# Kernel tuning notes

Hardware: AMD Instinct MI355X
Metric: run time of the kernel (lower is better)

Reference implementation:

```python
import jax, jax.numpy as jnp
import numpy as np

B, W, H, C = 8, 32, 32, 64   # batch, width, height, hidden_size
NH = 8                        # num_attention_heads
M = 32                        # max_position_embeddings
P = C // 2                    # position_embedding_size (query_positional_score=True)


def setup_inputs() -> dict:
    key = jax.random.key(0)
    ks = jax.random.split(key, 7)
    s = 0.02
    return {
        "hidden_states": jax.random.normal(ks[0], (B, W, H, C), dtype=jnp.float32),
        "row_emb": jax.random.normal(ks[1], (2 * M - 1, P), dtype=jnp.float32) * s,
        "col_emb": jax.random.normal(ks[2], (2 * M - 1, P), dtype=jnp.float32) * s,
        "Wq": jax.random.normal(ks[3], (NH * C, C), dtype=jnp.float32) * s,
        "bq": jnp.zeros((NH * C,), dtype=jnp.float32),
        "Wk": jax.random.normal(ks[4], (NH * C, C), dtype=jnp.float32) * s,
        "bk": jnp.zeros((NH * C,), dtype=jnp.float32),
        "Wv": jax.random.normal(ks[5], (C, NH * C), dtype=jnp.float32) * s,
        "bv": jnp.zeros((C,), dtype=jnp.float32),
    }


def reference(hidden_states, row_emb, col_emb, Wq, bq, Wk, bk, Wv, bv):
    b, w, h, c = hidden_states.shape
    nh = Wq.shape[0] // c
    half = c // 2
    center = row_emb.shape[0] // 2  # = max_position_embeddings - 1

    # projections: all_head_size = nh * c (per source: hidden_size * num_heads)
    q = (hidden_states @ Wq.T + bq).reshape(b, w, h, nh, c)
    k = (hidden_states @ Wk.T + bk).reshape(b, w, h, nh, c)

    # relative index tables: rel[i, j] = (j - i) + (M - 1)
    iw = jnp.arange(w)
    ih = jnp.arange(h)
    rel_w = iw[None, :] - iw[:, None] + center   # (w, w)
    rel_h = ih[None, :] - ih[:, None] + center   # (h, h)
    r_emb = row_emb[rel_w]  # (w, w, P)
    c_emb = col_emb[rel_h]  # (h, h, P)

    # positional scores: q split into row/col halves
    q_row = q[..., :half]
    q_col = q[..., half:]
    row_scores = jnp.einsum('bijhd,ikd->bijhk', q_row, r_emb)  # (b,w,h,nh,w)
    col_scores = jnp.einsum('bijhd,jld->bijhl', q_col, c_emb)  # (b,w,h,nh,h)
    scale = jnp.sqrt(jnp.asarray(c, dtype=hidden_states.dtype))
    scores = (row_scores[..., :, None] + col_scores[..., None, :]) / scale  # (b,w,h,nh,w,h)

    # content scores q^T k
    scores = scores + jnp.einsum('bijhd,bklhd->bijhkl', q, k) / scale

    # softmax over merged spatial key dims (k,l)
    probs = jax.nn.softmax(scores.reshape(b, w, h, nh, w * h), axis=-1).reshape(scores.shape)

    # value mixing directly with hidden_states, then output projection
    mixed = jnp.einsum('bijhkl,bkld->bijhd', probs, hidden_states).reshape(b, w, h, nh * c)
    return mixed @ Wv.T + bv
```

## Files before the change

kernel.cpp:

```cpp
#include <hip/hip_runtime.h>
#include <math.h>

typedef __bf16 bf16;
typedef bf16 bf16x2 __attribute__((ext_vector_type(2)));
typedef bf16 bf16x4 __attribute__((ext_vector_type(4)));
typedef bf16 bf16x8 __attribute__((ext_vector_type(8)));
typedef float f32x4 __attribute__((ext_vector_type(4)));

constexpr int CENTER = 31;
constexpr float QSCALE = 0.125f * 1.4426950408889634f;

static __device__ __forceinline__ unsigned short f2bf_bits(float f) {
    bf16 b = (bf16)f;
    return __builtin_bit_cast(unsigned short, b);
}

static __device__ __forceinline__ float fast_exp2(float x) {
#if __has_builtin(__builtin_amdgcn_exp2f)
    return __builtin_amdgcn_exp2f(x);
#else
    return exp2f(x);
#endif
}

__global__ __launch_bounds__(256)
void prep_kernel(const float* __restrict__ hid,
                 const float* __restrict__ Wq, const float* __restrict__ Wk,
                 const float* __restrict__ Wv,
                 bf16* __restrict__ hb, bf16* __restrict__ htb,
                 bf16* __restrict__ Wqb, bf16* __restrict__ Wkb,
                 bf16* __restrict__ Wvp)
{
    __shared__ __attribute__((aligned(16))) bf16 hs[64][72];

    const int t   = threadIdx.x;
    const int blk = blockIdx.x;
    const int b   = blk >> 4, kc = blk & 15;

    {
        int row = t >> 2, c4 = (t & 3) * 16;
        const float4* src = (const float4*)(hid + ((size_t)b * 1024 + kc * 64 + row) * 64 + c4);
        bf16 tmp[16];
        #pragma unroll
        for (int u = 0; u < 4; ++u) {
            float4 v = src[u];
            tmp[4*u+0] = (bf16)v.x; tmp[4*u+1] = (bf16)v.y;
            tmp[4*u+2] = (bf16)v.z; tmp[4*u+3] = (bf16)v.w;
        }
        *(int4*)&hs[row][c4]     = ((int4*)tmp)[0];
        *(int4*)&hs[row][c4 + 8] = ((int4*)tmp)[1];
        bf16* hdst = hb + ((size_t)b * 1024 + kc * 64 + row) * 64 + c4;
        *(int4*)hdst       = ((int4*)tmp)[0];
        *(int4*)(hdst + 8) = ((int4*)tmp)[1];
    }

    {
        int idx = blk * 256 + t;
        if (idx < 8192) {
            float4 vq = ((const float4*)Wq)[idx];
            float4 vk = ((const float4*)Wk)[idx];
            float4 vv = ((const float4*)Wv)[idx];
            ushort4 pq, pk2, pv;
            pq.x = f2bf_bits(vq.x); pq.y = f2bf_bits(vq.y); pq.z = f2bf_bits(vq.z); pq.w = f2bf_bits(vq.w);
            pk2.x = f2bf_bits(vk.x); pk2.y = f2bf_bits(vk.y); pk2.z = f2bf_bits(vk.z); pk2.w = f2bf_bits(vk.w);
            pv.x = f2bf_bits(vv.x); pv.y = f2bf_bits(vv.y); pv.z = f2bf_bits(vv.z); pv.w = f2bf_bits(vv.w);
            ((ushort4*)Wqb)[idx] = pq;
            ((ushort4*)Wkb)[idx] = pk2;
            int c = idx >> 7, o4 = (idx & 127) * 4;
            size_t dst = (size_t)((c >> 4) * 16 + (o4 >> 5)) * 512 + (c & 15) * 32 + (o4 & 31);
            *(ushort4*)(Wvp + dst) = pv;
        }
    }
    __syncthreads();

    {
        int d = t >> 2, p0 = (t & 3) * 16;
        ushort tmp[16];
        #pragma unroll
        for (int i = 0; i < 16; ++i)
            tmp[i] = __builtin_bit_cast(unsigned short, hs[p0 + i][d]);
        bf16* dst = htb + ((size_t)b * 64 + d) * 1024 + kc * 64 + p0;
        *(int4*)dst       = ((int4*)tmp)[0];
        *(int4*)(dst + 8) = ((int4*)tmp)[1];
    }
}

__global__ __launch_bounds__(256)
void qkproj_kernel(const bf16* __restrict__ hb,
                   const bf16* __restrict__ Wqb, const float* __restrict__ bq,
                   const bf16* __restrict__ Wkb, const float* __restrict__ bk,
                   bf16* __restrict__ qb, bf16* __restrict__ kb)
{
    __shared__ __attribute__((aligned(16))) bf16 As[128][72];
    __shared__ __attribute__((aligned(16))) bf16 Bs[128][72];

    const int t  = threadIdx.x;
    const int pt = blockIdx.x;
    const int ot = blockIdx.y;
    const int z  = blockIdx.z;
    const int p0 = pt * 128;
    const int b  = p0 >> 10;

    const bf16* Wb        = z ? Wkb : Wqb;
    const float* bias     = z ? bk : bq;
    bf16* outp            = z ? kb : qb;
    const float scale     = z ? 1.0f : QSCALE;

    {
        int row = t >> 1, ch = (t & 1) * 32;
        const int4* asrc = (const int4*)(hb + (size_t)(p0 + row) * 64 + ch);
        const int4* bsrc = (const int4*)(Wb + (size_t)(ot * 128 + row) * 64 + ch);
        #pragma unroll
        for (int u = 0; u < 4; ++u) {
            *(int4*)&As[row][ch + u * 8] = asrc[u];
            *(int4*)&Bs[row][ch + u * 8] = bsrc[u];
        }
    }
    __syncthreads();

    const int w = t >> 6, ln = t & 63, l15 = ln & 15, quad = ln >> 4;

    bf16x8 a[2][2];
    #pragma unroll
    for (int mt = 0; mt < 2; ++mt) {
        a[mt][0] = *(const bf16x8*)&As[w * 32 + mt * 16 + l15][quad * 8];
        a[mt][1] = *(const bf16x8*)&As[w * 32 + mt * 16 + l15][32 + quad * 8];
    }

    const f32x4 z4 = {0.f, 0.f, 0.f, 0.f};
    f32x4 acc[2][8];
    #pragma unroll
    for (int mt = 0; mt < 2; ++mt)
        #pragma unroll
        for (int nt = 0; nt < 8; ++nt) acc[mt][nt] = z4;

    #pragma unroll
    for (int nt = 0; nt < 8; ++nt) {
        bf16x8 b0 = *(const bf16x8*)&Bs[nt * 16 + l15][quad * 8];
        bf16x8 b1 = *(const bf16x8*)&Bs[nt * 16 + l15][32 + quad * 8];
        #pragma unroll
        for (int mt = 0; mt < 2; ++mt) {
            acc[mt][nt] = __builtin_amdgcn_mfma_f32_16x16x32_bf16(a[mt][0], b0, acc[mt][nt], 0, 0, 0);
            acc[mt][nt] = __builtin_amdgcn_mfma_f32_16x16x32_bf16(a[mt][1], b1, acc[mt][nt], 0, 0, 0);
        }
    }

    #pragma unroll
    for (int nt = 0; nt < 8; ++nt) {
        int o = ot * 128 + nt * 16 + l15;
        float bv = bias[o];
        int hh = o >> 6, d = o & 63;
        #pragma unroll
        for (int mt = 0; mt < 2; ++mt)
            #pragma unroll
            for (int r = 0; r < 4; ++r) {
                int pos = (p0 & 1023) + w * 32 + mt * 16 + quad * 4 + r;
                float val = (acc[mt][nt][r] + bv) * scale;
                outp[(((size_t)b * 8 + hh) * 1024 + pos) * 64 + d] = (bf16)val;
            }
    }
}

__global__ __launch_bounds__(256)
void bias_kernel(const bf16* __restrict__ qb,
                 const float* __restrict__ row_emb, const float* __restrict__ col_emb,
                 bf16* __restrict__ rowbias, bf16* __restrict__ colbias)
{
    __shared__ __attribute__((aligned(16))) bf16 embRs[63][40];
    __shared__ __attribute__((aligned(16))) bf16 embCs[63][40];

    const int t  = threadIdx.x;
    const int bh = blockIdx.x;
    const int sg = blockIdx.y;

    for (int i = t; i < 2016; i += 256) embRs[i >> 5][i & 31] = (bf16)row_emb[i];
    for (int i = t; i < 2016; i += 256) embCs[i >> 5][i & 31] = (bf16)col_emb[i];
    __syncthreads();

    const int w = t >> 6, ln = t & 63, l15 = ln & 15, quad = ln >> 4;

    #pragma unroll
    for (int u = 0; u < 2; ++u) {
        int s = sg * 8 + u * 4 + w;
        bool cm = s >= 32;
        int ij = cm ? s - 32 : s;

        bf16x8 a[2];
        #pragma unroll
        for (int mt = 0; mt < 2; ++mt) {
            const bf16* ap = cm
                ? qb + ((size_t)bh * 1024 + (mt * 16 + l15) * 32 + ij) * 64 + 32 + quad * 8
                : qb + ((size_t)bh * 1024 + ij * 32 + mt * 16 + l15) * 64 + quad * 8;
            a[mt] = *(const bf16x8*)ap;
        }
        bf16* ob = cm ? colbias : rowbias;

        #pragma unroll
        for (int nt = 0; nt < 2; ++nt) {
            int erow = nt * 16 + l15 + CENTER - ij;
            bf16x8 bfrag = cm ? *(const bf16x8*)&embCs[erow][quad * 8]
                              : *(const bf16x8*)&embRs[erow][quad * 8];
            #pragma unroll
            for (int mt = 0; mt < 2; ++mt) {
                f32x4 c = {0.f, 0.f, 0.f, 0.f};
                c = __builtin_amdgcn_mfma_f32_16x16x32_bf16(a[mt], bfrag, c, 0, 0, 0);
                #pragma unroll
                for (int r = 0; r < 4; ++r) {
                    int ql = mt * 16 + quad * 4 + r;
                    int qrow = cm ? ql * 32 + ij : ij * 32 + ql;
                    ob[((size_t)bh * 1024 + qrow) * 32 + nt * 16 + l15] = (bf16)c[r];
                }
            }
        }
    }
}

__global__ __launch_bounds__(256, 2)
void attn_kernel(const bf16* __restrict__ qb, const bf16* __restrict__ kb,
                 const bf16* __restrict__ htb,
                 const bf16* __restrict__ rowbias, const bf16* __restrict__ colbias,
                 bf16* __restrict__ mixedb)
{
    __shared__ __attribute__((aligned(16))) bf16 Ks[2][64][72];
    __shared__ __attribute__((aligned(16))) bf16 Hts[2][64][72];
    __shared__ __attribute__((aligned(16))) bf16 Pp[4][32][72];

    const int t  = threadIdx.x;
    const int id = blockIdx.x;
    const int r8 = id & 7;
    const int g  = id >> 3;
    const int qt = g & 7;
    const int bh = r8 * 8 + (g >> 3);
    const int b  = bh >> 3, h = bh & 7;
    const int q0 = qt * 128;
    const int w = t >> 6, ln = t & 63, l15 = ln & 15, quad = ln >> 4;

    bf16x8 bq_[2][2];
    float  cbv[2][2][4];
    const bf16* rbp[2];
    #pragma unroll
    for (int mt = 0; mt < 2; ++mt) {
        int qrow = q0 + w * 32 + mt * 16 + l15;
        const bf16* qp = qb + ((size_t)bh * 1024 + qrow) * 64;
        bq_[mt][0] = *(const bf16x8*)(qp + quad * 8);
        bq_[mt][1] = *(const bf16x8*)(qp + 32 + quad * 8);
        #pragma unroll
        for (int par = 0; par < 2; ++par) {
            bf16x4 cv = *(const bf16x4*)(colbias + ((size_t)bh * 1024 + qrow) * 32 + par * 16 + quad * 4);
            #pragma unroll
            for (int r = 0; r < 4; ++r) cbv[mt][par][r] = (float)cv[r];
        }
        rbp[mt] = rowbias + ((size_t)bh * 1024 + qrow) * 32;
    }

    const f32x4 z4 = {0.f, 0.f, 0.f, 0.f};
    f32x4 oacc[2][4];
    float lsum[2] = {0.f, 0.f};
    #pragma unroll
    for (int mt = 0; mt < 2; ++mt)
        #pragma unroll
        for (int dt = 0; dt < 4; ++dt) oacc[mt][dt] = z4;

    bf16* Pw = &Pp[w][0][0];
    const bf16* kcbase = kb + (size_t)bh * 1024 * 64;
    const bf16* hcbase = htb + (size_t)b * 64 * 1024;

    const int srow = t >> 2, sc = (t & 3) << 4;
    const bf16* kptr = kcbase + (size_t)srow * 64 + sc;
    const bf16* hptr = hcbase + (size_t)srow * 1024 + sc;

    int4 kr0 = *(const int4*)(kptr);
    int4 kr1 = *(const int4*)(kptr + 8);
    int4 hr0 = *(const int4*)(hptr);
    int4 hr1 = *(const int4*)(hptr + 8);
    *(int4*)&Ks[0][srow][sc]       = kr0;
    *(int4*)&Ks[0][srow][sc + 8]   = kr1;
    *(int4*)&Hts[0][srow][sc]      = hr0;
    *(int4*)&Hts[0][srow][sc + 8]  = hr1;
    kr0 = *(const int4*)(kptr + 4096);
    kr1 = *(const int4*)(kptr + 4096 + 8);
    hr0 = *(const int4*)(hptr + 64);
    hr1 = *(const int4*)(hptr + 64 + 8);
    bf16x2 rnext[2];
    #pragma unroll
    for (int mt = 0; mt < 2; ++mt) rnext[mt] = *(const bf16x2*)(rbp[mt]);
    __syncthreads();

    int cur = 0;
    for (int kc = 0; kc < 16; ++kc) {
        if (kc < 15) {
            *(int4*)&Ks[cur ^ 1][srow][sc]      = kr0;
            *(int4*)&Ks[cur ^ 1][srow][sc + 8]  = kr1;
            *(int4*)&Hts[cur ^ 1][srow][sc]     = hr0;
            *(int4*)&Hts[cur ^ 1][srow][sc + 8] = hr1;
        }
        float rb[2][2];
        #pragma unroll
        for (int mt = 0; mt < 2; ++mt) {
            rb[mt][0] = (float)rnext[mt][0];
            rb[mt][1] = (float)rnext[mt][1];
        }
        if (kc < 14) {
            const bf16* kn = kptr + (size_t)(kc + 2) * 4096;
            const bf16* hn = hptr + (size_t)(kc + 2) * 64;
            kr0 = *(const int4*)(kn);
            kr1 = *(const int4*)(kn + 8);
            hr0 = *(const int4*)(hn);
            hr1 = *(const int4*)(hn + 8);
        }
        if (kc < 15) {
            #pragma unroll
            for (int mt = 0; mt < 2; ++mt)
                rnext[mt] = *(const bf16x2*)(rbp[mt] + (kc + 1) * 2);
        }

        const bf16 (* __restrict__ Kc)[72]  = Ks[cur];
        const bf16 (* __restrict__ Hc)[72]  = Hts[cur];
        f32x4 sf[2][4];
        #pragma unroll
        for (int mt = 0; mt < 2; ++mt)
            #pragma unroll
            for (int kt = 0; kt < 4; ++kt) sf[mt][kt] = z4;
        __builtin_amdgcn_s_setprio(1);
        #pragma unroll
        for (int kt = 0; kt < 4; ++kt) {
            bf16x8 aK0 = *(const bf16x8*)&Kc[kt * 16 + l15][quad * 8];
            bf16x8 aK1 = *(const bf16x8*)&Kc[kt * 16 + l15][32 + quad * 8];
            #pragma unroll
            for (int mt = 0; mt < 2; ++mt) {
                sf[mt][kt] = __builtin_amdgcn_mfma_f32_16x16x32_bf16(aK0, bq_[mt][0], sf[mt][kt], 0, 0, 0);
                sf[mt][kt] = __builtin_amdgcn_mfma_f32_16x16x32_bf16(aK1, bq_[mt][1], sf[mt][kt], 0, 0, 0);
            }
        }
        __builtin_amdgcn_s_setprio(0);

        #pragma unroll
        for (int mt = 0; mt < 2; ++mt)
            #pragma unroll
            for (int kt = 0; kt < 4; ++kt) {
                float rbv = rb[mt][kt >> 1];
                ushort4 pk;
                float p0 = fast_exp2(sf[mt][kt][0] + rbv + cbv[mt][kt & 1][0]);
                float p1 = fast_exp2(sf[mt][kt][1] + rbv + cbv[mt][kt & 1][1]);
                float p2 = fast_exp2(sf[mt][kt][2] + rbv + cbv[mt][kt & 1][2]);
                float p3 = fast_exp2(sf[mt][kt][3] + rbv + cbv[mt][kt & 1][3]);
                lsum[mt] += (p0 + p1) + (p2 + p3);
                pk.x = f2bf_bits(p0); pk.y = f2bf_bits(p1);
                pk.z = f2bf_bits(p2); pk.w = f2bf_bits(p3);
                *(ushort4*)&Pw[(mt * 16 + l15) * 72 + kt * 16 + quad * 4] = pk;
            }

        bf16x8 bp[2][2];
        #pragma unroll
        for (int mt = 0; mt < 2; ++mt) {
            bp[mt][0] = *(const bf16x8*)&Pw[(mt * 16 + l15) * 72 + quad * 8];
            bp[mt][1] = *(const bf16x8*)&Pw[(mt * 16 + l15) * 72 + 32 + quad * 8];
        }
        __builtin_amdgcn_s_setprio(1);
        #pragma unroll
        for (int dt = 0; dt < 4; ++dt) {
            bf16x8 aH0 = *(const bf16x8*)&Hc[dt * 16 + l15][quad * 8];
            bf16x8 aH1 = *(const bf16x8*)&Hc[dt * 16 + l15][32 + quad * 8];
            #pragma unroll
            for (int mt = 0; mt < 2; ++mt) {
                oacc[mt][dt] = __builtin_amdgcn_mfma_f32_16x16x32_bf16(aH0, bp[mt][0], oacc[mt][dt], 0, 0, 0);
                oacc[mt][dt] = __builtin_amdgcn_mfma_f32_16x16x32_bf16(aH1, bp[mt][1], oacc[mt][dt], 0, 0, 0);
            }
        }
        __builtin_amdgcn_s_setprio(0);

        __syncthreads();
        cur ^= 1;
    }

    float inv[2];
    #pragma unroll
    for (int mt = 0; mt < 2; ++mt) {
        float v = lsum[mt];
        v += __shfl_xor(v, 16);
        v += __shfl_xor(v, 32);
        inv[mt] = 1.0f / v;
    }
    #pragma unroll
    for (int mt = 0; mt < 2; ++mt) {
        int pos = q0 + w * 32 + mt * 16 + l15;
        bf16* mb = mixedb + ((size_t)b * 1024 + pos) * 512 + h * 64;
        #pragma unroll
        for (int dt = 0; dt < 4; ++dt) {
            ushort4 pk;
            pk.x = f2bf_bits(oacc[mt][dt][0] * inv[mt]);
            pk.y = f2bf_bits(oacc[mt][dt][1] * inv[mt]);
            pk.z = f2bf_bits(oacc[mt][dt][2] * inv[mt]);
            pk.w = f2bf_bits(oacc[mt][dt][3] * inv[mt]);
            *(ushort4*)(mb + dt * 16 + quad * 4) = pk;
        }
    }
}

__global__ __launch_bounds__(256)
void out_proj_kernel(const bf16* __restrict__ mixedb,
                     const bf16* __restrict__ Wvp, const float* __restrict__ bv,
                     float* __restrict__ out)
{
    const int t  = threadIdx.x;
    const int p0 = blockIdx.x * 32;
    const int w = t >> 6, ln = t & 63, l15 = ln & 15, quad = ln >> 4;

    float bvv = bv[w * 16 + l15];
    f32x4 acc[2] = {(f32x4){bvv, bvv, bvv, bvv}, (f32x4){bvv, bvv, bvv, bvv}};

    const bf16* arow0 = mixedb + (size_t)(p0 + l15) * 512 + quad * 8;
    const bf16* arow1 = mixedb + (size_t)(p0 + 16 + l15) * 512 + quad * 8;
    const bf16* bbase = Wvp + (size_t)w * 16 * 512 + l15 * 32 + quad * 8;

    #pragma unroll
    for (int kc = 0; kc < 16; ++kc) {
        bf16x8 a0 = *(const bf16x8*)(arow0 + kc * 32);
        bf16x8 a1 = *(const bf16x8*)(arow1 + kc * 32);
        bf16x8 bfrag = *(const bf16x8*)(bbase + kc * 512);
        acc[0] = __builtin_amdgcn_mfma_f32_16x16x32_bf16(a0, bfrag, acc[0], 0, 0, 0);
        acc[1] = __builtin_amdgcn_mfma_f32_16x16x32_bf16(a1, bfrag, acc[1], 0, 0, 0);
    }

    #pragma unroll
    for (int mt = 0; mt < 2; ++mt)
        #pragma unroll
        for (int r = 0; r < 4; ++r)
            out[(size_t)(p0 + mt * 16 + quad * 4 + r) * 64 + w * 16 + l15] = acc[mt][r];
}

extern "C" void kernel_launch(void* const* d_in, const int* in_sizes, int n_in,
                              void* d_out, int out_size, void* d_ws, size_t ws_size,
                              hipStream_t stream)
{
    const float* hid     = (const float*)d_in[0];
    const float* row_emb = (const float*)d_in[1];
    const float* col_emb = (const float*)d_in[2];
    const float* Wq      = (const float*)d_in[3];
    const float* bq      = (const float*)d_in[4];
    const float* Wk      = (const float*)d_in[5];
    const float* bk      = (const float*)d_in[6];
    const float* Wv      = (const float*)d_in[7];
    const float* bv      = (const float*)d_in[8];
    float* out = (float*)d_out;

    bf16* qb      = (bf16*)d_ws;
    bf16* kb      = qb + (size_t)64 * 1024 * 64;
    bf16* htb     = kb + (size_t)64 * 1024 * 64;
    bf16* rowbias = htb + (size_t)8 * 64 * 1024;
    bf16* colbias = rowbias + (size_t)64 * 1024 * 32;
    bf16* mixedb  = colbias + (size_t)64 * 1024 * 32;
    bf16* hb      = mixedb + (size_t)8 * 1024 * 512;
    bf16* Wqb     = hb + (size_t)8 * 1024 * 64;
    bf16* Wkb     = Wqb + (size_t)512 * 64;
    bf16* Wvp     = Wkb + (size_t)512 * 64;

    prep_kernel<<<128, 256, 0, stream>>>(hid, Wq, Wk, Wv, hb, htb, Wqb, Wkb, Wvp);
    qkproj_kernel<<<dim3(64, 4, 2), 256, 0, stream>>>(hb, Wqb, bq, Wkb, bk, qb, kb);
    bias_kernel<<<dim3(64, 8), 256, 0, stream>>>(qb, row_emb, col_emb, rowbias, colbias);
    attn_kernel<<<512, 256, 0, stream>>>(qb, kb, htb, rowbias, colbias, mixedb);
    out_proj_kernel<<<256, 256, 0, stream>>>(mixedb, Wvp, bv, out);
}
```

Measured before the change: 131.3 us.

## Fuse prep and QK projection kernels, seed MFMA accumulators with bias

Merges the fp32-to-bf16 prep kernel into the QK projection kernel. Projection blocks now read fp32 hidden states and weights directly and convert them while staging into shared memory. Extra blocks in the same grid build the transposed hidden tensor and the packed Wv. This removes one launch and the intermediate bf16 hb/Wqb/Wkb buffers, but projection blocks now read twice as many input bytes. Separately, the attention kernel starts its score accumulators at the row and column bias, which removes the adds before exp2.

```diff
diff --git a/kernel.cpp b/kernel.cpp
--- a/kernel.cpp
+++ b/kernel.cpp
@@ -24,96 +24,91 @@
 }
 
 __global__ __launch_bounds__(256)
-void prep_kernel(const float* __restrict__ hid,
-                 const float* __restrict__ Wq, const float* __restrict__ Wk,
-                 const float* __restrict__ Wv,
-                 bf16* __restrict__ hb, bf16* __restrict__ htb,
-                 bf16* __restrict__ Wqb, bf16* __restrict__ Wkb,
-                 bf16* __restrict__ Wvp)
+void prep_qkproj_kernel(const float* __restrict__ hid,
+                        const float* __restrict__ Wq, const float* __restrict__ bq,
+                        const float* __restrict__ Wk, const float* __restrict__ bk,
+                        const float* __restrict__ Wv,
+                        bf16* __restrict__ qb, bf16* __restrict__ kb,
+                        bf16* __restrict__ htb, bf16* __restrict__ Wvp)
 {
-    __shared__ __attribute__((aligned(16))) bf16 hs[64][72];
-
-    const int t   = threadIdx.x;
-    const int blk = blockIdx.x;
-    const int b   = blk >> 4, kc = blk & 15;
-
-    {
-        int row = t >> 2, c4 = (t & 3) * 16;
-        const float4* src = (const float4*)(hid + ((size_t)b * 1024 + kc * 64 + row) * 64 + c4);
-        bf16 tmp[16];
-        #pragma unroll
-        for (int u = 0; u < 4; ++u) {
-            float4 v = src[u];
-            tmp[4*u+0] = (bf16)v.x; tmp[4*u+1] = (bf16)v.y;
-            tmp[4*u+2] = (bf16)v.z; tmp[4*u+3] = (bf16)v.w;
-        }
-        *(int4*)&hs[row][c4]     = ((int4*)tmp)[0];
-        *(int4*)&hs[row][c4 + 8] = ((int4*)tmp)[1];
-        bf16* hdst = hb + ((size_t)b * 1024 + kc * 64 + row) * 64 + c4;
-        *(int4*)hdst       = ((int4*)tmp)[0];
-        *(int4*)(hdst + 8) = ((int4*)tmp)[1];
-    }
-
-    {
-        int idx = blk * 256 + t;
-        if (idx < 8192) {
-            float4 vq = ((const float4*)Wq)[idx];
-            float4 vk = ((const float4*)Wk)[idx];
-            float4 vv = ((const float4*)Wv)[idx];
-            ushort4 pq, pk2, pv;
-            pq.x = f2bf_bits(vq.x); pq.y = f2bf_bits(vq.y); pq.z = f2bf_bits(vq.z); pq.w = f2bf_bits(vq.w);
-            pk2.x = f2bf_bits(vk.x); pk2.y = f2bf_bits(vk.y); pk2.z = f2bf_bits(vk.z); pk2.w = f2bf_bits(vk.w);
-            pv.x = f2bf_bits(vv.x); pv.y = f2bf_bits(vv.y); pv.z = f2bf_bits(vv.z); pv.w = f2bf_bits(vv.w);
-            ((ushort4*)Wqb)[idx] = pq;
-            ((ushort4*)Wkb)[idx] = pk2;
-            int c = idx >> 7, o4 = (idx & 127) * 4;
-            size_t dst = (size_t)((c >> 4) * 16 + (o4 >> 5)) * 512 + (c & 15) * 32 + (o4 & 31);
-            *(ushort4*)(Wvp + dst) = pv;
-        }
-    }
-    __syncthreads();
-
-    {
-        int d = t >> 2, p0 = (t & 3) * 16;
-        ushort tmp[16];
-        #pragma unroll
-        for (int i = 0; i < 16; ++i)
-            tmp[i] = __builtin_bit_cast(unsigned short, hs[p0 + i][d]);
-        bf16* dst = htb + ((size_t)b * 64 + d) * 1024 + kc * 64 + p0;
-        *(int4*)dst       = ((int4*)tmp)[0];
-        *(int4*)(dst + 8) = ((int4*)tmp)[1];
-    }
-}
-
-__global__ __launch_bounds__(256)
-void qkproj_kernel(const bf16* __restrict__ hb,
-                   const bf16* __restrict__ Wqb, const float* __restrict__ bq,
-                   const bf16* __restrict__ Wkb, const float* __restrict__ bk,
-                   bf16* __restrict__ qb, bf16* __restrict__ kb)
-{
+    const int id = blockIdx.x;
+    const int t  = threadIdx.x;
+
+    if (id >= 512) {
+        __shared__ __attribute__((aligned(16))) bf16 hs[64][72];
+        const int pb = id - 512;
+        const int b  = pb >> 4, kc = pb & 15;
+
+        {
+            int row = t >> 2, c4 = (t & 3) * 16;
+            const float4* src = (const float4*)(hid + ((size_t)b * 1024 + kc * 64 + row) * 64 + c4);
+            bf16 tmp[16];
+            #pragma unroll
+            for (int u = 0; u < 4; ++u) {
+                float4 v = src[u];
+                tmp[4*u+0] = (bf16)v.x; tmp[4*u+1] = (bf16)v.y;
+                tmp[4*u+2] = (bf16)v.z; tmp[4*u+3] = (bf16)v.w;
+            }
+            *(int4*)&hs[row][c4]     = ((int4*)tmp)[0];
+            *(int4*)&hs[row][c4 + 8] = ((int4*)tmp)[1];
+        }
+        {
+            int idx = pb * 256 + t;
+            if (idx < 8192) {
+                float4 vv = ((const float4*)Wv)[idx];
+                ushort4 pv;
+                pv.x = f2bf_bits(vv.x); pv.y = f2bf_bits(vv.y);
+                pv.z = f2bf_bits(vv.z); pv.w = f2bf_bits(vv.w);
+                int c = idx >> 7, o4 = (idx & 127) * 4;
+                size_t dst = (size_t)((c >> 4) * 16 + (o4 >> 5)) * 512 + (c & 15) * 32 + (o4 & 31);
+                *(ushort4*)(Wvp + dst) = pv;
+            }
+        }
+        __syncthreads();
+        {
+            int d = t >> 2, p0 = (t & 3) * 16;
+            ushort tmp[16];
+            #pragma unroll
+            for (int i = 0; i < 16; ++i)
+                tmp[i] = __builtin_bit_cast(unsigned short, hs[p0 + i][d]);
+            bf16* dst = htb + ((size_t)b * 64 + d) * 1024 + kc * 64 + p0;
+            *(int4*)dst       = ((int4*)tmp)[0];
+            *(int4*)(dst + 8) = ((int4*)tmp)[1];
+        }
+        return;
+    }
+
     __shared__ __attribute__((aligned(16))) bf16 As[128][72];
     __shared__ __attribute__((aligned(16))) bf16 Bs[128][72];
 
-    const int t  = threadIdx.x;
-    const int pt = blockIdx.x;
-    const int ot = blockIdx.y;
-    const int z  = blockIdx.z;
+    const int pt = id & 63;
+    const int ot = (id >> 6) & 3;
+    const int z  = (id >> 8) & 1;
     const int p0 = pt * 128;
     const int b  = p0 >> 10;
 
-    const bf16* Wb        = z ? Wkb : Wqb;
-    const float* bias     = z ? bk : bq;
-    bf16* outp            = z ? kb : qb;
-    const float scale     = z ? 1.0f : QSCALE;
+    const float* Wsrc  = z ? Wk : Wq;
+    const float* bias  = z ? bk : bq;
+    bf16* outp         = z ? kb : qb;
+    const float scale  = z ? 1.0f : QSCALE;
 
     {
         int row = t >> 1, ch = (t & 1) * 32;
-        const int4* asrc = (const int4*)(hb + (size_t)(p0 + row) * 64 + ch);
-        const int4* bsrc = (const int4*)(Wb + (size_t)(ot * 128 + row) * 64 + ch);
+        const float4* asrc = (const float4*)(hid + (size_t)(p0 + row) * 64 + ch);
+        const float4* bsrc = (const float4*)(Wsrc + (size_t)(ot * 128 + row) * 64 + ch);
+        bf16 ta[32], tb[32];
+        #pragma unroll
+        for (int u = 0; u < 8; ++u) {
+            float4 va = asrc[u], vb = bsrc[u];
+            ta[4*u+0] = (bf16)va.x; ta[4*u+1] = (bf16)va.y;
+            ta[4*u+2] = (bf16)va.z; ta[4*u+3] = (bf16)va.w;
+            tb[4*u+0] = (bf16)vb.x; tb[4*u+1] = (bf16)vb.y;
+            tb[4*u+2] = (bf16)vb.z; tb[4*u+3] = (bf16)vb.w;
+        }
         #pragma unroll
         for (int u = 0; u < 4; ++u) {
-            *(int4*)&As[row][ch + u * 8] = asrc[u];
-            *(int4*)&Bs[row][ch + u * 8] = bsrc[u];
+            *(int4*)&As[row][ch + u * 8] = ((int4*)ta)[u];
+            *(int4*)&Bs[row][ch + u * 8] = ((int4*)tb)[u];
         }
     }
     __syncthreads();
@@ -320,7 +315,12 @@
         #pragma unroll
         for (int mt = 0; mt < 2; ++mt)
             #pragma unroll
-            for (int kt = 0; kt < 4; ++kt) sf[mt][kt] = z4;
+            for (int kt = 0; kt < 4; ++kt) {
+                float rbv = rb[mt][kt >> 1];
+                #pragma unroll
+                for (int r = 0; r < 4; ++r)
+                    sf[mt][kt][r] = rbv + cbv[mt][kt & 1][r];
+            }
         __builtin_amdgcn_s_setprio(1);
         #pragma unroll
         for (int kt = 0; kt < 4; ++kt) {
@@ -338,12 +338,11 @@
         for (int mt = 0; mt < 2; ++mt)
             #pragma unroll
             for (int kt = 0; kt < 4; ++kt) {
-                float rbv = rb[mt][kt >> 1];
                 ushort4 pk;
-                float p0 = fast_exp2(sf[mt][kt][0] + rbv + cbv[mt][kt & 1][0]);
-                float p1 = fast_exp2(sf[mt][kt][1] + rbv + cbv[mt][kt & 1][1]);
-                float p2 = fast_exp2(sf[mt][kt][2] + rbv + cbv[mt][kt & 1][2]);
-                float p3 = fast_exp2(sf[mt][kt][3] + rbv + cbv[mt][kt & 1][3]);
+                float p0 = fast_exp2(sf[mt][kt][0]);
+                float p1 = fast_exp2(sf[mt][kt][1]);
+                float p2 = fast_exp2(sf[mt][kt][2]);
+                float p3 = fast_exp2(sf[mt][kt][3]);
                 lsum[mt] += (p0 + p1) + (p2 + p3);
                 pk.x = f2bf_bits(p0); pk.y = f2bf_bits(p1);
                 pk.z = f2bf_bits(p2); pk.w = f2bf_bits(p3);
@@ -450,13 +449,9 @@
     bf16* rowbias = htb + (size_t)8 * 64 * 1024;
     bf16* colbias = rowbias + (size_t)64 * 1024 * 32;
     bf16* mixedb  = colbias + (size_t)64 * 1024 * 32;
-    bf16* hb      = mixedb + (size_t)8 * 1024 * 512;
-    bf16* Wqb     = hb + (size_t)8 * 1024 * 64;
-    bf16* Wkb     = Wqb + (size_t)512 * 64;
-    bf16* Wvp     = Wkb + (size_t)512 * 64;
-
-    prep_kernel<<<128, 256, 0, stream>>>(hid, Wq, Wk, Wv, hb, htb, Wqb, Wkb, Wvp);
-    qkproj_kernel<<<dim3(64, 4, 2), 256, 0, stream>>>(hb, Wqb, bq, Wkb, bk, qb, kb);
+    bf16* Wvp     = mixedb + (size_t)8 * 1024 * 512;
+
+    prep_qkproj_kernel<<<640, 256, 0, stream>>>(hid, Wq, bq, Wk, bk, Wv, qb, kb, htb, Wvp);
     bias_kernel<<<dim3(64, 8), 256, 0, stream>>>(qb, row_emb, col_emb, rowbias, colbias);
     attn_kernel<<<512, 256, 0, stream>>>(qb, kb, htb, rowbias, colbias, mixedb);
     out_proj_kernel<<<256, 256, 0, stream>>>(mixedb, Wvp, bv, out);
```

After: 128.0 us. 2.5% less time.
